# Optimization experiments

Hardware: AMD Instinct MI355X
Metric: run time of the kernel (lower is better)

The kernel has to match this reference:

```python
import jax, jax.numpy as jnp
import numpy as np

N, E, B, V, ED, M = 100000, 1600000, 100, 10000, 16, 64
EPS = 1e-5

def _seg_mean(x, ids, n):
    s = jax.ops.segment_sum(x, ids, num_segments=n)
    c = jax.ops.segment_sum(jnp.ones((x.shape[0], 1), x.dtype), ids, num_segments=n)
    return s / jnp.maximum(c, 1.0)

def _graph_conv(x, src, dst, ew, w_rel, b_rel, w_root):
    # PyG GraphConv: out = lin_rel(sum_j e_ji * x_j) + lin_root(x)
    msg = x[src] * ew[:, None]                       # [E, din] gather + weight
    agg = jax.ops.segment_sum(msg, dst, num_segments=x.shape[0])  # scatter-add
    return agg @ w_rel + b_rel + x @ w_root

def _graph_norm(x, batch, g, b, a):
    m = _seg_mean(x, batch, B)
    xc = x - a * m[batch]
    v = _seg_mean(xc * xc, batch, B)
    return g * xc / jnp.sqrt(v[batch] + EPS) + b

def _lrelu(x):
    return jnp.where(x > 0, x, 0.01 * x)

def _bn(x, g, b):
    m = x.mean(0)
    v = x.var(0)
    return g * (x - m) / jnp.sqrt(v + EPS) + b

def setup_inputs() -> dict:
    key = jax.random.key(0)
    ks = jax.random.split(key, 36)
    def lin(k, din, dout):
        return jax.random.normal(k, (din, dout), jnp.float32) / np.sqrt(din)
    d = {
        'x_idx': jax.random.randint(ks[0], (N,), 0, V),
        'edge_index': jax.random.randint(ks[1], (2, E), 0, N),
        'edge_attr': jax.random.uniform(ks[2], (E, 1), jnp.float32),
        'batch': jnp.sort(jax.random.randint(ks[3], (N,), 0, B)),
        'demographics': jax.random.normal(ks[4], (B, 4), jnp.float32),
        'emb': jax.random.normal(ks[5], (V, ED), jnp.float32),
        'w_rel1': lin(ks[6], ED, M),   'b_rel1': jnp.zeros((M,), jnp.float32),   'w_root1': lin(ks[7], ED, M),
        'w_rel2': lin(ks[8], M, 2*M),  'b_rel2': jnp.zeros((2*M,), jnp.float32), 'w_root2': lin(ks[9], M, 2*M),
        'w_rel3': lin(ks[10], 2*M, 4*M),'b_rel3': jnp.zeros((4*M,), jnp.float32),'w_root3': lin(ks[11], 2*M, 4*M),
        'gn1_g': jnp.ones((M,), jnp.float32),   'gn1_b': jnp.zeros((M,), jnp.float32),   'gn1_a': jnp.ones((M,), jnp.float32),
        'gn2_g': jnp.ones((2*M,), jnp.float32), 'gn2_b': jnp.zeros((2*M,), jnp.float32), 'gn2_a': jnp.ones((2*M,), jnp.float32),
        'demo_w': lin(ks[12], 4, 16), 'demo_b': jnp.zeros((16,), jnp.float32),
        'l1_w': lin(ks[13], 4*M + 16, 2*M), 'l1_b': jnp.zeros((2*M,), jnp.float32),
        'bn1_g': jnp.ones((2*M,), jnp.float32), 'bn1_b': jnp.zeros((2*M,), jnp.float32),
        'l2_w': lin(ks[14], 2*M, M), 'l2_b': jnp.zeros((M,), jnp.float32),
        'bn2_g': jnp.ones((M,), jnp.float32), 'bn2_b': jnp.zeros((M,), jnp.float32),
        'l3_w': lin(ks[15], M, 3), 'l3_b': jnp.zeros((3,), jnp.float32),
    }
    return d

def reference(x_idx, edge_index, edge_attr, batch, demographics, emb,
              w_rel1, b_rel1, w_root1, w_rel2, b_rel2, w_root2, w_rel3, b_rel3, w_root3,
              gn1_g, gn1_b, gn1_a, gn2_g, gn2_b, gn2_a,
              demo_w, demo_b, l1_w, l1_b, bn1_g, bn1_b, l2_w, l2_b, bn2_g, bn2_b, l3_w, l3_b):
    src, dst = edge_index[0], edge_index[1]
    ew = edge_attr[:, 0]                  # squeeze(-1)
    x = emb[x_idx]                        # [N, 16]
    x = _graph_conv(x, src, dst, ew, w_rel1, b_rel1, w_root1)
    x = _lrelu(_graph_norm(x, batch, gn1_g, gn1_b, gn1_a))
    x = _graph_conv(x, src, dst, ew, w_rel2, b_rel2, w_root2)
    x = _lrelu(_graph_norm(x, batch, gn2_g, gn2_b, gn2_a))
    x = _graph_conv(x, src, dst, ew, w_rel3, b_rel3, w_root3)   # [N, 256]
    gf = _seg_mean(x, batch, B)                                  # global_mean_pool [B, 256]
    demo = demographics @ demo_w + demo_b                        # [B, 16]
    h = jnp.concatenate([gf, demo], axis=1)                      # [B, 272]
    h = _lrelu(_bn(h @ l1_w + l1_b, bn1_g, bn1_b))               # dropout = identity (eval)
    h = _lrelu(_bn(h @ l2_w + l2_b, bn2_g, bn2_b))
    return h @ l3_w + l3_b                                       # [B, 3]
```

## Files before the change

### kernel.cpp

```cpp
#include <hip/hip_runtime.h>

#define NN 100000
#define NE 1600000
#define NBATCH 100
#define NBUCK 391
constexpr float EPS = 1e-5f;

typedef unsigned short ushort_t;
typedef unsigned int uint_t;

using short8 = __attribute__((ext_vector_type(8))) short;
using floatx4 = __attribute__((ext_vector_type(4))) float;

__device__ __forceinline__ float lrelu(float x) { return x > 0.f ? x : 0.01f * x; }

__device__ __forceinline__ float b2f(ushort_t u) {
    union { uint_t i; float f; } c; c.i = ((uint_t)u) << 16; return c.f;
}
__device__ __forceinline__ ushort_t f2b(float f) {
    union { float f; uint_t i; } c; c.f = f;
    uint_t u = c.i;
    return (ushort_t)((u + 0x7FFFu + ((u >> 16) & 1u)) >> 16);
}
__device__ __forceinline__ void unpack8(const uint4 u, float* f) {
    f[0] = b2f(u.x & 0xffff); f[1] = b2f(u.x >> 16);
    f[2] = b2f(u.y & 0xffff); f[3] = b2f(u.y >> 16);
    f[4] = b2f(u.z & 0xffff); f[5] = b2f(u.z >> 16);
    f[6] = b2f(u.w & 0xffff); f[7] = b2f(u.w >> 16);
}


__global__ __launch_bounds__(256) void k_bcount(const int* __restrict__ dst,
                                                int* __restrict__ bcnt) {
    __shared__ int h[NBUCK];
    for (int i = threadIdx.x; i < NBUCK; i += 256) h[i] = 0;
    __syncthreads();
    for (int e = blockIdx.x * 256 + threadIdx.x; e < NE; e += gridDim.x * 256)
        atomicAdd(&h[dst[e] >> 8], 1);
    __syncthreads();
    for (int i = threadIdx.x; i < NBUCK; i += 256)
        if (h[i]) atomicAdd(&bcnt[i], h[i]);
}

__global__ __launch_bounds__(512) void k_bscan(const int* __restrict__ bcnt,
                                               int* __restrict__ bbase,
                                               int* __restrict__ bcur,
                                               int* __restrict__ rowstart) {
    __shared__ int s[512];
    const int t = threadIdx.x;
    const int v = (t < NBUCK) ? bcnt[t] : 0;
    s[t] = v;
    __syncthreads();
    for (int off = 1; off < 512; off <<= 1) {
        int o = (t >= off) ? s[t - off] : 0;
        __syncthreads();
        s[t] += o;
        __syncthreads();
    }
    const int excl = s[t] - v;
    if (t < NBUCK) { bbase[t] = excl; bcur[t] = excl; }
    if (t == 0) { bbase[NBUCK] = NE; rowstart[NN] = NE; }
}

__global__ __launch_bounds__(256) void k_bscatter(const int* __restrict__ dst,
                                                  const int* __restrict__ srcv,
                                                  const float* __restrict__ ew,
                                                  int* __restrict__ bcur,
                                                  int2* __restrict__ ebuf) {
    __shared__ int h[NBUCK];
    __shared__ int lcur[NBUCK];
    const int chunk = (NE + gridDim.x - 1) / gridDim.x;
    const int beg = blockIdx.x * chunk;
    const int end = (beg + chunk < NE) ? beg + chunk : NE;
    for (int i = threadIdx.x; i < NBUCK; i += 256) h[i] = 0;
    __syncthreads();
    for (int e = beg + threadIdx.x; e < end; e += 256)
        atomicAdd(&h[dst[e] >> 8], 1);
    __syncthreads();
    for (int i = threadIdx.x; i < NBUCK; i += 256)
        lcur[i] = h[i] ? atomicAdd(&bcur[i], h[i]) : 0;
    __syncthreads();
    for (int e = beg + threadIdx.x; e < end; e += 256) {
        const int d = dst[e];
        const int pos = atomicAdd(&lcur[d >> 8], 1);
        ebuf[pos] = make_int2(srcv[e] | ((d & 255) << 20), __float_as_int(ew[e]));
    }
}

__global__ __launch_bounds__(256) void k_bfinal(const int2* __restrict__ ebuf,
                                                const int* __restrict__ bbase,
                                                int* __restrict__ rowstart,
                                                int2* __restrict__ csr_pair) {
    __shared__ int h[256];
    __shared__ int cur[256];
    const int b = blockIdx.x;
    const int t = threadIdx.x;
    const int base = bbase[b];
    const int cnt = bbase[b + 1] - base;
    h[t] = 0;
    __syncthreads();
    for (int i = t; i < cnt; i += 256)
        atomicAdd(&h[(ebuf[base + i].x >> 20) & 255], 1);
    __syncthreads();
    const int v = h[t];
    cur[t] = v;
    __syncthreads();
    for (int off = 1; off < 256; off <<= 1) {
        int o = (t >= off) ? cur[t - off] : 0;
        __syncthreads();
        cur[t] += o;
        __syncthreads();
    }
    const int excl = cur[t] - v;
    const int n = (b << 8) + t;
    if (n < NN) rowstart[n] = base + excl;
    __syncthreads();
    cur[t] = excl;
    __syncthreads();
    for (int i = t; i < cnt; i += 256) {
        const int2 p = ebuf[base + i];
        const int loc = (p.x >> 20) & 255;
        const int pos = base + atomicAdd(&cur[loc], 1);
        csr_pair[pos] = make_int2(p.x & 0xFFFFF, p.y);
    }
}

__global__ void k_bounds(const int* __restrict__ batch, int* __restrict__ bstart) {
    int b = blockIdx.x * blockDim.x + threadIdx.x;
    if (b > NBATCH) return;
    int lo = 0, hi = NN;
    while (lo < hi) {
        int mid = (lo + hi) >> 1;
        if (batch[mid] < b) lo = mid + 1; else hi = mid;
    }
    bstart[b] = lo;
}


__global__ void k_wpack(const float* __restrict__ wr1, const float* __restrict__ wo1,
                        const float* __restrict__ wr2, const float* __restrict__ wo2,
                        const float* __restrict__ wr3, const float* __restrict__ wo3,
                        ushort_t* __restrict__ w1T, ushort_t* __restrict__ w2T,
                        ushort_t* __restrict__ w3T) {
    int idx = blockIdx.x * blockDim.x + threadIdx.x;
    if (idx < 2048) {
        int n = idx >> 5, k = idx & 31;
        float v = (k < 16) ? wr1[k * 64 + n] : wo1[(k - 16) * 64 + n];
        w1T[idx] = f2b(v);
    } else if (idx < 2048 + 16384) {
        int l = idx - 2048; int n = l >> 7, k = l & 127;
        float v = (k < 64) ? wr2[k * 128 + n] : wo2[(k - 64) * 128 + n];
        w2T[l] = f2b(v);
    } else if (idx < 2048 + 16384 + 65536) {
        int l = idx - 18432; int n = l >> 8, k = l & 255;
        float v = (k < 128) ? wr3[k * 256 + n] : wo3[(k - 128) * 256 + n];
        w3T[l] = f2b(v);
    }
}


__global__ void k_gather_b(const int* __restrict__ xi, const float* __restrict__ emb,
                           ushort_t* __restrict__ xcat0) {
    int n = blockIdx.x * blockDim.x + threadIdx.x;
    if (n >= NN) return;
    const float* e = emb + ((size_t)xi[n] << 4);
    uint_t u[8];
#pragma unroll
    for (int j = 0; j < 8; ++j)
        u[j] = (uint_t)f2b(e[2 * j]) | ((uint_t)f2b(e[2 * j + 1]) << 16);
    uint4* o = (uint4*)(xcat0 + (size_t)n * 32 + 16);
    o[0] = {u[0], u[1], u[2], u[3]};
    o[1] = {u[4], u[5], u[6], u[7]};
}


template <int D>
__global__ void k_aggregate_b(ushort_t* __restrict__ xcat, const int2* __restrict__ csr_pair,
                              const int* __restrict__ rowstart) {
    constexpr int LPN = D / 8;
    constexpr int EP = 64 / LPN;
    const int n = blockIdx.x * 4 + (threadIdx.x >> 6);
    const int lane = threadIdx.x & 63;
    const int sl = lane % LPN;
    const int eg = lane / LPN;
    if (n >= NN) return;
    const int beg = rowstart[n], end = rowstart[n + 1];
    float a0[8] = {}, a1[8] = {};
    int i = beg + eg;
    for (; i + EP < end; i += 2 * EP) {
        const int2 p0 = csr_pair[i];
        const int2 p1 = csr_pair[i + EP];
        const float w0 = __int_as_float(p0.y);
        const float w1 = __int_as_float(p1.y);
        const uint4 u0 = *(const uint4*)(xcat + (size_t)p0.x * (2 * D) + D + sl * 8);
        const uint4 u1 = *(const uint4*)(xcat + (size_t)p1.x * (2 * D) + D + sl * 8);
        float f0[8], f1[8];
        unpack8(u0, f0); unpack8(u1, f1);
#pragma unroll
        for (int j = 0; j < 8; ++j) { a0[j] += f0[j] * w0; a1[j] += f1[j] * w1; }
    }
    if (i < end) {
        const int2 p0 = csr_pair[i];
        const float w0 = __int_as_float(p0.y);
        const uint4 u0 = *(const uint4*)(xcat + (size_t)p0.x * (2 * D) + D + sl * 8);
        float f0[8];
        unpack8(u0, f0);
#pragma unroll
        for (int j = 0; j < 8; ++j) a0[j] += f0[j] * w0;
    }
#pragma unroll
    for (int j = 0; j < 8; ++j) a0[j] += a1[j];
#pragma unroll
    for (int m = LPN; m < 64; m <<= 1)
#pragma unroll
        for (int j = 0; j < 8; ++j) a0[j] += __shfl_xor(a0[j], m);
    if (eg == 0) {
        uint_t u[4];
#pragma unroll
        for (int j = 0; j < 4; ++j)
            u[j] = (uint_t)f2b(a0[2 * j]) | ((uint_t)f2b(a0[2 * j + 1]) << 16);
        *(uint4*)(xcat + (size_t)n * (2 * D) + sl * 8) = {u[0], u[1], u[2], u[3]};
    }
}


template <int K2, int DOUT, int MODE>
__global__ __launch_bounds__(256) void k_conv_mfma(
        const ushort_t* __restrict__ xcat, const ushort_t* __restrict__ wcatT,
        const float* __restrict__ brel, float* __restrict__ outp,
        const int* __restrict__ batch, const int* __restrict__ bstart,
        float* __restrict__ gfacc) {
    constexpr int CW = DOUT / 64;
    const int lane = threadIdx.x & 63;
    const int wv = threadIdx.x >> 6;
    const int m = lane & 15;
    const int quad = lane >> 4;
    const int r0 = blockIdx.x * 64;

    floatx4 acc[4][CW] = {};

    const ushort_t* arow[4];
#pragma unroll
    for (int r = 0; r < 4; ++r) {
        int an = r0 + r * 16 + m; if (an >= NN) an = NN - 1;
        arow[r] = xcat + (size_t)an * K2 + quad * 8;
    }
    const ushort_t* brow[CW];
#pragma unroll
    for (int c = 0; c < CW; ++c)
        brow[c] = wcatT + (size_t)((wv * CW + c) * 16 + m) * K2 + quad * 8;

    for (int kk = 0; kk < K2; kk += 32) {
        short8 a[4], b[CW];
#pragma unroll
        for (int r = 0; r < 4; ++r) a[r] = *(const short8*)(arow[r] + kk);
#pragma unroll
        for (int c = 0; c < CW; ++c) b[c] = *(const short8*)(brow[c] + kk);
#pragma unroll
        for (int r = 0; r < 4; ++r)
#pragma unroll
            for (int c = 0; c < CW; ++c)
                acc[r][c] = __builtin_amdgcn_mfma_f32_16x16x32_bf16(a[r], b[c], acc[r][c], 0, 0, 0);
    }

    float bias[CW];
#pragma unroll
    for (int c = 0; c < CW; ++c) bias[c] = brel[(wv * CW + c) * 16 + m];

    if constexpr (MODE == 0) {
#pragma unroll
        for (int c = 0; c < CW; ++c) {
            const int col = (wv * CW + c) * 16 + m;
#pragma unroll
            for (int r = 0; r < 4; ++r)
#pragma unroll
                for (int rr = 0; rr < 4; ++rr) {
                    const int row = r0 + r * 16 + quad * 4 + rr;
                    if (row < NN)
                        outp[(size_t)row * DOUT + col] = acc[r][c][rr] + bias[c];
                }
        }
    } else {
        const int rtop = (r0 + 63 < NN) ? r0 + 63 : NN - 1;
        const int sb0 = batch[r0];
        const int sb1 = batch[rtop];
        for (int sb = sb0; sb <= sb1; ++sb) {
            const int lo = (bstart[sb] > r0) ? bstart[sb] : r0;
            int hi = bstart[sb + 1];
            if (hi > r0 + 64) hi = r0 + 64;
            float s[CW];
#pragma unroll
            for (int c = 0; c < CW; ++c) s[c] = 0.f;
#pragma unroll
            for (int r = 0; r < 4; ++r)
#pragma unroll
                for (int rr = 0; rr < 4; ++rr) {
                    const int row = r0 + r * 16 + quad * 4 + rr;
                    if (row >= lo && row < hi) {
#pragma unroll
                        for (int c = 0; c < CW; ++c) s[c] += acc[r][c][rr] + bias[c];
                    }
                }
#pragma unroll
            for (int c = 0; c < CW; ++c) {
                s[c] += __shfl_xor(s[c], 16);
                s[c] += __shfl_xor(s[c], 32);
            }
            if (quad == 0) {
#pragma unroll
                for (int c = 0; c < CW; ++c)
                    atomicAdd(&gfacc[sb * 256 + (wv * CW + c) * 16 + m], s[c]);
            }
        }
    }
}

__global__ void k_gffin(const float* __restrict__ gfacc, const int* __restrict__ bstart,
                        float* __restrict__ h0) {
    int idx = blockIdx.x * blockDim.x + threadIdx.x;
    if (idx >= NBATCH * 256) return;
    int b = idx >> 8, c = idx & 255;
    float cnt = fmaxf((float)(bstart[b + 1] - bstart[b]), 1.f);
    h0[b * 272 + c] = gfacc[idx] / cnt;
}


template <int D, int OST>
__global__ __launch_bounds__(256) void k_graphnorm(
        const float* __restrict__ xf, ushort_t* __restrict__ xout,
        const int* __restrict__ bstart, const float* __restrict__ a,
        const float* __restrict__ g, const float* __restrict__ bb) {
    __shared__ float4 reds[256];
    __shared__ float4 redq[256];
    __shared__ float smean[64];
    __shared__ float sinv[64];
    const int b = blockIdx.x;
    const int col0 = blockIdx.y * 64;
    const int c4 = (threadIdx.x & 15) * 4;
    const int rg = threadIdx.x >> 4;
    const int beg = bstart[b], end = bstart[b + 1];
    const float cntf = fmaxf((float)(end - beg), 1.f);

    float4 s = {0.f, 0.f, 0.f, 0.f}, q = {0.f, 0.f, 0.f, 0.f};
    for (int r = beg + rg; r < end; r += 16) {
        const float4 v = *(const float4*)&xf[(size_t)r * D + col0 + c4];
        s.x += v.x; s.y += v.y; s.z += v.z; s.w += v.w;
        q.x += v.x * v.x; q.y += v.y * v.y; q.z += v.z * v.z; q.w += v.w * v.w;
    }
    reds[threadIdx.x] = s;
    redq[threadIdx.x] = q;
    __syncthreads();
    if (rg == 0) {
        float4 S = reds[threadIdx.x], Q = redq[threadIdx.x];
        for (int k = 1; k < 16; ++k) {
            const float4 s2 = reds[threadIdx.x + 16 * k];
            const float4 q2 = redq[threadIdx.x + 16 * k];
            S.x += s2.x; S.y += s2.y; S.z += s2.z; S.w += s2.w;
            Q.x += q2.x; Q.y += q2.y; Q.z += q2.z; Q.w += q2.w;
        }
        const float4 al = *(const float4*)&a[col0 + c4];
        const float Sv[4] = {S.x, S.y, S.z, S.w};
        const float Qv[4] = {Q.x, Q.y, Q.z, Q.w};
        const float av[4] = {al.x, al.y, al.z, al.w};
#pragma unroll
        for (int c = 0; c < 4; ++c) {
            const float mm = Sv[c] / cntf;
            const float ex2 = Qv[c] / cntf;
            const float var = fmaxf(ex2 - mm * mm * (2.f * av[c] - av[c] * av[c]), 0.f);
            smean[c4 + c] = mm;
            sinv[c4 + c] = 1.f / sqrtf(var + EPS);
        }
    }
    __syncthreads();
    const float4 mean4 = *(const float4*)&smean[c4];
    const float4 inv4 = *(const float4*)&sinv[c4];
    const float4 al4 = *(const float4*)&a[col0 + c4];
    const float4 g4 = *(const float4*)&g[col0 + c4];
    const float4 bb4 = *(const float4*)&bb[col0 + c4];
    for (int r = beg + rg; r < end; r += 16) {
        const float4 v = *(const float4*)&xf[(size_t)r * D + col0 + c4];
        float y0 = lrelu(g4.x * (v.x - al4.x * mean4.x) * inv4.x + bb4.x);
        float y1 = lrelu(g4.y * (v.y - al4.y * mean4.y) * inv4.y + bb4.y);
        float y2 = lrelu(g4.z * (v.z - al4.z * mean4.z) * inv4.z + bb4.z);
        float y3 = lrelu(g4.w * (v.w - al4.w * mean4.w) * inv4.w + bb4.w);
        uint2 o;
        o.x = (uint_t)f2b(y0) | ((uint_t)f2b(y1) << 16);
        o.y = (uint_t)f2b(y2) | ((uint_t)f2b(y3) << 16);
        *(uint2*)&xout[(size_t)r * OST + col0 + c4] = o;
    }
}

__global__ void k_demo(const float* __restrict__ dg, const float* __restrict__ w,
                       const float* __restrict__ b, float* __restrict__ h0) {
    int idx = blockIdx.x * blockDim.x + threadIdx.x;
    if (idx < NBATCH * 16) {
        int i = idx >> 4, j = idx & 15;
        float acc = b[j];
        for (int k = 0; k < 4; ++k) acc += dg[i * 4 + k] * w[k * 16 + j];
        h0[i * 272 + 256 + j] = acc;
    }
}


template <int K, int C>
__global__ __launch_bounds__(C) void k_head_lin(const float* __restrict__ in,
                                                const float* __restrict__ w,
                                                const float* __restrict__ bias,
                                                float* __restrict__ z, int rows) {
    __shared__ float s_in[16][K];
    const int j = threadIdx.x;
    const int r0 = blockIdx.x * 16;
    for (int idx = threadIdx.x; idx < 16 * K; idx += C) {
        int r = idx / K, k = idx - r * K;
        s_in[r][k] = (r0 + r < rows) ? in[(size_t)(r0 + r) * K + k] : 0.f;
    }
    __syncthreads();
    float acc[16];
#pragma unroll
    for (int r = 0; r < 16; ++r) acc[r] = 0.f;
    for (int k = 0; k < K; ++k) {
        const float wv = w[k * C + j];
#pragma unroll
        for (int r = 0; r < 16; ++r) acc[r] += s_in[r][k] * wv;
    }
    const float bj = bias[j];
#pragma unroll
    for (int r = 0; r < 16; ++r)
        if (r0 + r < rows) z[(size_t)(r0 + r) * C + j] = acc[r] + bj;
}

__global__ void k_head_bn(float* __restrict__ z, const float* __restrict__ g,
                          const float* __restrict__ b, int rows, int C) {
    const int j = threadIdx.x;
    if (j >= C) return;
    float s = 0.f, q = 0.f;
    for (int i = 0; i < rows; ++i) { const float v = z[i * C + j]; s += v; q += v * v; }
    const float m = s / rows;
    const float var = fmaxf(q / rows - m * m, 0.f);
    const float inv = 1.f / sqrtf(var + EPS);
    const float gg = g[j], bb = b[j];
    for (int i = 0; i < rows; ++i)
        z[i * C + j] = lrelu(gg * (z[i * C + j] - m) * inv + bb);
}

__global__ __launch_bounds__(256) void k_head_out(const float* __restrict__ h2,
                                                  const float* __restrict__ w,
                                                  const float* __restrict__ b,
                                                  float* __restrict__ out) {
    __shared__ float s[NBATCH * 65];
    for (int idx = threadIdx.x; idx < NBATCH * 64; idx += 256) {
        int i = idx >> 6, k = idx & 63;
        s[i * 65 + k] = h2[idx];
    }
    __syncthreads();
    const int i = threadIdx.x;
    if (i < NBATCH) {
        float a0 = b[0], a1 = b[1], a2 = b[2];
        for (int k = 0; k < 64; ++k) {
            const float v = s[i * 65 + k];
            a0 += v * w[k * 3 + 0];
            a1 += v * w[k * 3 + 1];
            a2 += v * w[k * 3 + 2];
        }
        out[i * 3 + 0] = a0; out[i * 3 + 1] = a1; out[i * 3 + 2] = a2;
    }
}


extern "C" void kernel_launch(void* const* d_in, const int* in_sizes, int n_in,
                              void* d_out, int out_size, void* d_ws, size_t ws_size,
                              hipStream_t stream) {
    const int*   x_idx  = (const int*)d_in[0];
    const int*   ei     = (const int*)d_in[1];
    const float* eattr  = (const float*)d_in[2];
    const int*   batch  = (const int*)d_in[3];
    const float* demog  = (const float*)d_in[4];
    const float* emb    = (const float*)d_in[5];
    const float* wrel1  = (const float*)d_in[6];
    const float* brel1  = (const float*)d_in[7];
    const float* wroot1 = (const float*)d_in[8];
    const float* wrel2  = (const float*)d_in[9];
    const float* brel2  = (const float*)d_in[10];
    const float* wroot2 = (const float*)d_in[11];
    const float* wrel3  = (const float*)d_in[12];
    const float* brel3  = (const float*)d_in[13];
    const float* wroot3 = (const float*)d_in[14];
    const float* gn1g = (const float*)d_in[15];
    const float* gn1b = (const float*)d_in[16];
    const float* gn1a = (const float*)d_in[17];
    const float* gn2g = (const float*)d_in[18];
    const float* gn2b = (const float*)d_in[19];
    const float* gn2a = (const float*)d_in[20];
    const float* dw   = (const float*)d_in[21];
    const float* db   = (const float*)d_in[22];
    const float* l1w  = (const float*)d_in[23];
    const float* l1b  = (const float*)d_in[24];
    const float* bn1g = (const float*)d_in[25];
    const float* bn1b = (const float*)d_in[26];
    const float* l2w  = (const float*)d_in[27];
    const float* l2b  = (const float*)d_in[28];
    const float* bn2g = (const float*)d_in[29];
    const float* bn2b = (const float*)d_in[30];
    const float* l3w  = (const float*)d_in[31];
    const float* l3b  = (const float*)d_in[32];
    float* out = (float*)d_out;

    float*    W     = (float*)d_ws;
    float*    xf    = W;
    int2*     ebuf  = (int2*)W;
    float*    gfacc = W + 12800000;
    ushort_t* xcat0 = (ushort_t*)(W + 25600000);
    ushort_t* xcat1 = (ushort_t*)(W + 27200000);
    ushort_t* xcat2 = (ushort_t*)(W + 33600000);
    ushort_t* w1T   = (ushort_t*)(W + 46400000);
    ushort_t* w2T   = w1T + 2048;
    ushort_t* w3T   = w2T + 16384;
    int2*     csr_pair = (int2*)(W + 46450000);
    int*      rowstart = (int*)(W + 49650000);
    int*      bstart   = (int*)(W + 49760000);
    int*      bcnt     = (int*)(W + 49761000);
    int*      bbase    = (int*)(W + 49762000);
    int*      bcur     = (int*)(W + 49763000);
    float*    h0 = W + 49770000;
    float*    h1 = h0 + 27200;
    float*    h2 = h1 + 12800;

    const int* src = ei;
    const int* dst = ei + NE;

    const int mfma_blk = (NN + 63) / 64;
    const int nagg_blk = (NN + 3) / 4;

    hipMemsetAsync(bcnt, 0, NBUCK * sizeof(int), stream);
    k_bcount<<<256, 256, 0, stream>>>(dst, bcnt);
    k_bscan<<<1, 512, 0, stream>>>(bcnt, bbase, bcur, rowstart);
    k_bscatter<<<256, 256, 0, stream>>>(dst, src, eattr, bcur, ebuf);
    k_bfinal<<<NBUCK, 256, 0, stream>>>(ebuf, bbase, rowstart, csr_pair);

    k_bounds<<<1, 128, 0, stream>>>(batch, bstart);
    k_wpack<<<(83968 + 255) / 256, 256, 0, stream>>>(wrel1, wroot1, wrel2, wroot2, wrel3, wroot3,
                                                     w1T, w2T, w3T);
    hipMemsetAsync(gfacc, 0, NBATCH * 256 * sizeof(float), stream);

    k_gather_b<<<(NN + 255) / 256, 256, 0, stream>>>(x_idx, emb, xcat0);

    k_aggregate_b<16><<<nagg_blk, 256, 0, stream>>>(xcat0, csr_pair, rowstart);
    k_conv_mfma<32, 64, 0><<<mfma_blk, 256, 0, stream>>>(xcat0, w1T, brel1, xf, batch, bstart, nullptr);
    k_graphnorm<64, 128><<<dim3(NBATCH, 1), 256, 0, stream>>>(xf, xcat1 + 64, bstart, gn1a, gn1g, gn1b);

    k_aggregate_b<64><<<nagg_blk, 256, 0, stream>>>(xcat1, csr_pair, rowstart);
    k_conv_mfma<128, 128, 0><<<mfma_blk, 256, 0, stream>>>(xcat1, w2T, brel2, xf, batch, bstart, nullptr);
    k_graphnorm<128, 256><<<dim3(NBATCH, 2), 256, 0, stream>>>(xf, xcat2 + 128, bstart, gn2a, gn2g, gn2b);

    k_aggregate_b<128><<<nagg_blk, 256, 0, stream>>>(xcat2, csr_pair, rowstart);
    k_conv_mfma<256, 256, 2><<<mfma_blk, 256, 0, stream>>>(xcat2, w3T, brel3, nullptr, batch, bstart, gfacc);

    k_gffin<<<(NBATCH * 256 + 255) / 256, 256, 0, stream>>>(gfacc, bstart, h0);
    k_demo<<<(NBATCH * 16 + 255) / 256, 256, 0, stream>>>(demog, dw, db, h0);
    k_head_lin<272, 128><<<(NBATCH + 15) / 16, 128, 0, stream>>>(h0, l1w, l1b, h1, NBATCH);
    k_head_bn<<<1, 128, 0, stream>>>(h1, bn1g, bn1b, NBATCH, 128);
    k_head_lin<128, 64><<<(NBATCH + 15) / 16, 64, 0, stream>>>(h1, l2w, l2b, h2, NBATCH);
    k_head_bn<<<1, 64, 0, stream>>>(h2, bn2g, bn2b, NBATCH, 64);
    k_head_out<<<1, 256, 0, stream>>>(h2, l3w, l3b, out);
}
```

Baseline: 662.9 us.

## Fuse graphnorm stats into conv epilogue and aggregate layer 3 from fp8

The conv MFMA epilogue now accumulates per-graph sum and sum-of-squares with atomics, so the graphnorm kernel no longer makes a separate reduction pass over the activations and only applies the normalization. The layer-2 graphnorm also writes an fp8 copy of its output, and the layer-3 edge aggregation gathers neighbor features from that fp8 buffer instead of bf16, halving gather bytes. This adds atomics and extra memsets, and lowers the precision of the largest gather, which may affect accuracy.

```diff
diff --git a/kernel.cpp b/kernel.cpp
--- a/kernel.cpp
+++ b/kernel.cpp
@@ -8,9 +8,11 @@
 
 typedef unsigned short ushort_t;
 typedef unsigned int uint_t;
+typedef unsigned char uchar_t;
 
 using short8 = __attribute__((ext_vector_type(8))) short;
 using floatx4 = __attribute__((ext_vector_type(4))) float;
+using floatx2 = __attribute__((ext_vector_type(2))) float;
 
 __device__ __forceinline__ float lrelu(float x) { return x > 0.f ? x : 0.01f * x; }
 
@@ -27,6 +29,14 @@
     f[2] = b2f(u.y & 0xffff); f[3] = b2f(u.y >> 16);
     f[4] = b2f(u.z & 0xffff); f[5] = b2f(u.z >> 16);
     f[6] = b2f(u.w & 0xffff); f[7] = b2f(u.w >> 16);
+}
+__device__ __forceinline__ void unpack8_f8(const uint2 u, float* f) {
+    floatx2 a = __builtin_amdgcn_cvt_pk_f32_fp8(u.x, false);
+    floatx2 b = __builtin_amdgcn_cvt_pk_f32_fp8(u.x, true);
+    floatx2 c = __builtin_amdgcn_cvt_pk_f32_fp8(u.y, false);
+    floatx2 d = __builtin_amdgcn_cvt_pk_f32_fp8(u.y, true);
+    f[0] = a[0]; f[1] = a[1]; f[2] = b[0]; f[3] = b[1];
+    f[4] = c[0]; f[5] = c[1]; f[6] = d[0]; f[7] = d[1];
 }
 
 
@@ -224,12 +234,62 @@
 }
 
 
+__global__ void k_aggregate_f8(ushort_t* __restrict__ xcat, const uchar_t* __restrict__ x8,
+                               const int2* __restrict__ csr_pair, const int* __restrict__ rowstart) {
+    constexpr int D = 128;
+    constexpr int LPN = 16;
+    constexpr int EP = 4;
+    const int n = blockIdx.x * 4 + (threadIdx.x >> 6);
+    const int lane = threadIdx.x & 63;
+    const int sl = lane % LPN;
+    const int eg = lane / LPN;
+    if (n >= NN) return;
+    const int beg = rowstart[n], end = rowstart[n + 1];
+    float a0[8] = {}, a1[8] = {};
+    int i = beg + eg;
+    for (; i + EP < end; i += 2 * EP) {
+        const int2 p0 = csr_pair[i];
+        const int2 p1 = csr_pair[i + EP];
+        const float w0 = __int_as_float(p0.y);
+        const float w1 = __int_as_float(p1.y);
+        const uint2 u0 = *(const uint2*)(x8 + (size_t)p0.x * D + sl * 8);
+        const uint2 u1 = *(const uint2*)(x8 + (size_t)p1.x * D + sl * 8);
+        float f0[8], f1[8];
+        unpack8_f8(u0, f0); unpack8_f8(u1, f1);
+#pragma unroll
+        for (int j = 0; j < 8; ++j) { a0[j] += f0[j] * w0; a1[j] += f1[j] * w1; }
+    }
+    if (i < end) {
+        const int2 p0 = csr_pair[i];
+        const float w0 = __int_as_float(p0.y);
+        const uint2 u0 = *(const uint2*)(x8 + (size_t)p0.x * D + sl * 8);
+        float f0[8];
+        unpack8_f8(u0, f0);
+#pragma unroll
+        for (int j = 0; j < 8; ++j) a0[j] += f0[j] * w0;
+    }
+#pragma unroll
+    for (int j = 0; j < 8; ++j) a0[j] += a1[j];
+#pragma unroll
+    for (int m = LPN; m < 64; m <<= 1)
+#pragma unroll
+        for (int j = 0; j < 8; ++j) a0[j] += __shfl_xor(a0[j], m);
+    if (eg == 0) {
+        uint_t u[4];
+#pragma unroll
+        for (int j = 0; j < 4; ++j)
+            u[j] = (uint_t)f2b(a0[2 * j]) | ((uint_t)f2b(a0[2 * j + 1]) << 16);
+        *(uint4*)(xcat + (size_t)n * (2 * D) + sl * 8) = {u[0], u[1], u[2], u[3]};
+    }
+}
+
+
 template <int K2, int DOUT, int MODE>
 __global__ __launch_bounds__(256) void k_conv_mfma(
         const ushort_t* __restrict__ xcat, const ushort_t* __restrict__ wcatT,
         const float* __restrict__ brel, float* __restrict__ outp,
         const int* __restrict__ batch, const int* __restrict__ bstart,
-        float* __restrict__ gfacc) {
+        float* __restrict__ sacc, float* __restrict__ qacc) {
     constexpr int CW = DOUT / 64;
     const int lane = threadIdx.x & 63;
     const int wv = threadIdx.x >> 6;
@@ -267,7 +327,7 @@
 #pragma unroll
     for (int c = 0; c < CW; ++c) bias[c] = brel[(wv * CW + c) * 16 + m];
 
-    if constexpr (MODE == 0) {
+    if constexpr (MODE == 1) {
 #pragma unroll
         for (int c = 0; c < CW; ++c) {
             const int col = (wv * CW + c) * 16 + m;
@@ -279,6 +339,43 @@
                     if (row < NN)
                         outp[(size_t)row * DOUT + col] = acc[r][c][rr] + bias[c];
                 }
+        }
+        const int rtop = (r0 + 63 < NN) ? r0 + 63 : NN - 1;
+        const int sb0 = batch[r0];
+        const int sb1 = batch[rtop];
+        for (int sb = sb0; sb <= sb1; ++sb) {
+            const int lo = (bstart[sb] > r0) ? bstart[sb] : r0;
+            int hi = bstart[sb + 1];
+            if (hi > r0 + 64) hi = r0 + 64;
+            float s[CW], q[CW];
+#pragma unroll
+            for (int c = 0; c < CW; ++c) { s[c] = 0.f; q[c] = 0.f; }
+#pragma unroll
+            for (int r = 0; r < 4; ++r)
+#pragma unroll
+                for (int rr = 0; rr < 4; ++rr) {
+                    const int row = r0 + r * 16 + quad * 4 + rr;
+                    if (row >= lo && row < hi) {
+#pragma unroll
+                        for (int c = 0; c < CW; ++c) {
+                            const float v = acc[r][c][rr] + bias[c];
+                            s[c] += v; q[c] += v * v;
+                        }
+                    }
+                }
+#pragma unroll
+            for (int c = 0; c < CW; ++c) {
+                s[c] += __shfl_xor(s[c], 16); s[c] += __shfl_xor(s[c], 32);
+                q[c] += __shfl_xor(q[c], 16); q[c] += __shfl_xor(q[c], 32);
+            }
+            if (quad == 0) {
+#pragma unroll
+                for (int c = 0; c < CW; ++c) {
+                    const int col = (wv * CW + c) * 16 + m;
+                    atomicAdd(&sacc[sb * DOUT + col], s[c]);
+                    atomicAdd(&qacc[sb * DOUT + col], q[c]);
+                }
+            }
         }
     } else {
         const int rtop = (r0 + 63 < NN) ? r0 + 63 : NN - 1;
@@ -309,7 +406,7 @@
             if (quad == 0) {
 #pragma unroll
                 for (int c = 0; c < CW; ++c)
-                    atomicAdd(&gfacc[sb * 256 + (wv * CW + c) * 16 + m], s[c]);
+                    atomicAdd(&sacc[sb * 256 + (wv * CW + c) * 16 + m], s[c]);
             }
         }
     }
@@ -325,15 +422,12 @@
 }
 
 
-template <int D, int OST>
-__global__ __launch_bounds__(256) void k_graphnorm(
-        const float* __restrict__ xf, ushort_t* __restrict__ xout,
-        const int* __restrict__ bstart, const float* __restrict__ a,
+template <int D, int OST, bool F8>
+__global__ __launch_bounds__(256) void k_gnapply(
+        const float* __restrict__ xf, ushort_t* __restrict__ xout, uchar_t* __restrict__ x8out,
+        const int* __restrict__ bstart, const float* __restrict__ sacc,
+        const float* __restrict__ qacc, const float* __restrict__ a,
         const float* __restrict__ g, const float* __restrict__ bb) {
-    __shared__ float4 reds[256];
-    __shared__ float4 redq[256];
-    __shared__ float smean[64];
-    __shared__ float sinv[64];
     const int b = blockIdx.x;
     const int col0 = blockIdx.y * 64;
     const int c4 = (threadIdx.x & 15) * 4;
@@ -341,52 +435,38 @@
     const int beg = bstart[b], end = bstart[b + 1];
     const float cntf = fmaxf((float)(end - beg), 1.f);
 
-    float4 s = {0.f, 0.f, 0.f, 0.f}, q = {0.f, 0.f, 0.f, 0.f};
-    for (int r = beg + rg; r < end; r += 16) {
-        const float4 v = *(const float4*)&xf[(size_t)r * D + col0 + c4];
-        s.x += v.x; s.y += v.y; s.z += v.z; s.w += v.w;
-        q.x += v.x * v.x; q.y += v.y * v.y; q.z += v.z * v.z; q.w += v.w * v.w;
-    }
-    reds[threadIdx.x] = s;
-    redq[threadIdx.x] = q;
-    __syncthreads();
-    if (rg == 0) {
-        float4 S = reds[threadIdx.x], Q = redq[threadIdx.x];
-        for (int k = 1; k < 16; ++k) {
-            const float4 s2 = reds[threadIdx.x + 16 * k];
-            const float4 q2 = redq[threadIdx.x + 16 * k];
-            S.x += s2.x; S.y += s2.y; S.z += s2.z; S.w += s2.w;
-            Q.x += q2.x; Q.y += q2.y; Q.z += q2.z; Q.w += q2.w;
-        }
-        const float4 al = *(const float4*)&a[col0 + c4];
-        const float Sv[4] = {S.x, S.y, S.z, S.w};
-        const float Qv[4] = {Q.x, Q.y, Q.z, Q.w};
-        const float av[4] = {al.x, al.y, al.z, al.w};
-#pragma unroll
-        for (int c = 0; c < 4; ++c) {
-            const float mm = Sv[c] / cntf;
-            const float ex2 = Qv[c] / cntf;
-            const float var = fmaxf(ex2 - mm * mm * (2.f * av[c] - av[c] * av[c]), 0.f);
-            smean[c4 + c] = mm;
-            sinv[c4 + c] = 1.f / sqrtf(var + EPS);
-        }
-    }
-    __syncthreads();
-    const float4 mean4 = *(const float4*)&smean[c4];
-    const float4 inv4 = *(const float4*)&sinv[c4];
+    const float4 S = *(const float4*)&sacc[b * D + col0 + c4];
+    const float4 Q = *(const float4*)&qacc[b * D + col0 + c4];
     const float4 al4 = *(const float4*)&a[col0 + c4];
     const float4 g4 = *(const float4*)&g[col0 + c4];
     const float4 bb4 = *(const float4*)&bb[col0 + c4];
+    float mean[4], inv[4];
+    const float Sv[4] = {S.x, S.y, S.z, S.w};
+    const float Qv[4] = {Q.x, Q.y, Q.z, Q.w};
+    const float av[4] = {al4.x, al4.y, al4.z, al4.w};
+#pragma unroll
+    for (int c = 0; c < 4; ++c) {
+        const float mm = Sv[c] / cntf;
+        const float ex2 = Qv[c] / cntf;
+        const float var = fmaxf(ex2 - mm * mm * (2.f * av[c] - av[c] * av[c]), 0.f);
+        mean[c] = mm;
+        inv[c] = 1.f / sqrtf(var + EPS);
+    }
     for (int r = beg + rg; r < end; r += 16) {
         const float4 v = *(const float4*)&xf[(size_t)r * D + col0 + c4];
-        float y0 = lrelu(g4.x * (v.x - al4.x * mean4.x) * inv4.x + bb4.x);
-        float y1 = lrelu(g4.y * (v.y - al4.y * mean4.y) * inv4.y + bb4.y);
-        float y2 = lrelu(g4.z * (v.z - al4.z * mean4.z) * inv4.z + bb4.z);
-        float y3 = lrelu(g4.w * (v.w - al4.w * mean4.w) * inv4.w + bb4.w);
+        const float y0 = lrelu(g4.x * (v.x - av[0] * mean[0]) * inv[0] + bb4.x);
+        const float y1 = lrelu(g4.y * (v.y - av[1] * mean[1]) * inv[1] + bb4.y);
+        const float y2 = lrelu(g4.z * (v.z - av[2] * mean[2]) * inv[2] + bb4.z);
+        const float y3 = lrelu(g4.w * (v.w - av[3] * mean[3]) * inv[3] + bb4.w);
         uint2 o;
         o.x = (uint_t)f2b(y0) | ((uint_t)f2b(y1) << 16);
         o.y = (uint_t)f2b(y2) | ((uint_t)f2b(y3) << 16);
         *(uint2*)&xout[(size_t)r * OST + col0 + c4] = o;
+        if constexpr (F8) {
+            uint_t p = __builtin_amdgcn_cvt_pk_fp8_f32(y0, y1, 0, false);
+            p = __builtin_amdgcn_cvt_pk_fp8_f32(y2, y3, p, true);
+            *(uint_t*)&x8out[(size_t)r * D + col0 + c4] = p;
+        }
     }
 }
 
@@ -524,6 +604,11 @@
     float*    h0 = W + 49770000;
     float*    h1 = h0 + 27200;
     float*    h2 = h1 + 12800;
+    float*    sacc1 = W + 49817000;
+    float*    qacc1 = sacc1 + 6400;
+    float*    sacc2 = W + 49830000;
+    float*    qacc2 = sacc2 + 12800;
+    uchar_t*  x8    = (uchar_t*)(W + 49860000);
 
     const int* src = ei;
     const int* dst = ei + NE;
@@ -541,19 +626,23 @@
     k_wpack<<<(83968 + 255) / 256, 256, 0, stream>>>(wrel1, wroot1, wrel2, wroot2, wrel3, wroot3,
                                                      w1T, w2T, w3T);
     hipMemsetAsync(gfacc, 0, NBATCH * 256 * sizeof(float), stream);
+    hipMemsetAsync(sacc1, 0, (6400 * 2) * sizeof(float), stream);
+    hipMemsetAsync(sacc2, 0, (12800 * 2) * sizeof(float), stream);
 
     k_gather_b<<<(NN + 255) / 256, 256, 0, stream>>>(x_idx, emb, xcat0);
 
     k_aggregate_b<16><<<nagg_blk, 256, 0, stream>>>(xcat0, csr_pair, rowstart);
-    k_conv_mfma<32, 64, 0><<<mfma_blk, 256, 0, stream>>>(xcat0, w1T, brel1, xf, batch, bstart, nullptr);
-    k_graphnorm<64, 128><<<dim3(NBATCH, 1), 256, 0, stream>>>(xf, xcat1 + 64, bstart, gn1a, gn1g, gn1b);
+    k_conv_mfma<32, 64, 1><<<mfma_blk, 256, 0, stream>>>(xcat0, w1T, brel1, xf, batch, bstart, sacc1, qacc1);
+    k_gnapply<64, 128, false><<<dim3(NBATCH, 1), 256, 0, stream>>>(xf, xcat1 + 64, nullptr,
+                                                                   bstart, sacc1, qacc1, gn1a, gn1g, gn1b);
 
     k_aggregate_b<64><<<nagg_blk, 256, 0, stream>>>(xcat1, csr_pair, rowstart);
-    k_conv_mfma<128, 128, 0><<<mfma_blk, 256, 0, stream>>>(xcat1, w2T, brel2, xf, batch, bstart, nullptr);
-    k_graphnorm<128, 256><<<dim3(NBATCH, 2), 256, 0, stream>>>(xf, xcat2 + 128, bstart, gn2a, gn2g, gn2b);
-
-    k_aggregate_b<128><<<nagg_blk, 256, 0, stream>>>(xcat2, csr_pair, rowstart);
-    k_conv_mfma<256, 256, 2><<<mfma_blk, 256, 0, stream>>>(xcat2, w3T, brel3, nullptr, batch, bstart, gfacc);
+    k_conv_mfma<128, 128, 1><<<mfma_blk, 256, 0, stream>>>(xcat1, w2T, brel2, xf, batch, bstart, sacc2, qacc2);
+    k_gnapply<128, 256, true><<<dim3(NBATCH, 2), 256, 0, stream>>>(xf, xcat2 + 128, x8,
+                                                                   bstart, sacc2, qacc2, gn2a, gn2g, gn2b);
+
+    k_aggregate_f8<<<nagg_blk, 256, 0, stream>>>(xcat2, x8, csr_pair, rowstart);
+    k_conv_mfma<256, 256, 2><<<mfma_blk, 256, 0, stream>>>(xcat2, w3T, brel3, nullptr, batch, bstart, gfacc, nullptr);
 
     k_gffin<<<(NBATCH * 256 + 255) / 256, 256, 0, stream>>>(gfacc, bstart, h0);
     k_demo<<<(NBATCH * 16 + 255) / 256, 256, 0, stream>>>(demog, dw, db, h0);
```

Measured after the change: 650.2 us. About the same (-1.9%).
